# Kernel optimization log

Hardware: AMD Instinct MI355X
Metric: run time of the kernel (lower is better)

Reference implementation:

```python
import jax, jax.numpy as jnp
import numpy as np
import math

B, T, C, TF, N, DK = 4, 2048, 768, 128, 8, 96  # DK = max(C//8,16)

def _tau_init(Tw):
    alpha = 0.1 ** (1.0 / max(Tw - 1, 1))
    tau = -math.log(max(alpha, 1e-10))
    return math.log(math.exp(tau) - 1 + 1e-10)

def setup_inputs() -> dict:
    key = jax.random.key(0)
    ks = jax.random.split(key, 13)
    w = lambda k, shp: jax.random.normal(k, shp, jnp.float32) * 0.02
    return {
        'x': jax.random.normal(ks[0], (B, T, C), jnp.float32),
        'tau_gate': jnp.float32(_tau_init(max(T // 2, 4))),
        'tau_fast': jnp.float32(_tau_init(TF)),
        'tau_slow': jnp.float32(_tau_init(T)),
        'Wp': w(ks[1], (C, C)), 'bp': jnp.zeros((C,), jnp.float32),
        'Wxf': w(ks[2], (C, C)), 'bxf': jnp.full((C,), -0.5, jnp.float32),
        'Wxs': w(ks[3], (C, C)), 'bxs': jnp.full((C,), 0.5, jnp.float32),
        'Wcf': w(ks[4], (C, C)), 'Wcs': w(ks[5], (C, C)),
        'Wq': w(ks[6], (DK, C)), 'Wk': w(ks[7], (DK, C)),
        'Wfast': w(ks[8], (C, C)), 'bfast': jnp.zeros((C,), jnp.float32),
        'Wslow': w(ks[9], (C, C)), 'bslow': jnp.zeros((C,), jnp.float32),
        'Wsoma': w(ks[10], (C, C)), 'bsoma': jnp.zeros((C,), jnp.float32),
        'Wanc': w(ks[11], (C, C)), 'banc': jnp.zeros((C,), jnp.float32),
        'anchor_scales': jnp.linspace(1.5, -1.5, N).astype(jnp.float32),
        'blend_raw': jnp.zeros((1,), jnp.float32),
        'ln_g': jnp.ones((C,), jnp.float32), 'ln_b': jnp.zeros((C,), jnp.float32),
    }

def _lin(x, W, b=None):
    # torch Linear: y = x @ W.T + b, W is (out, in)
    y = jnp.einsum('btc,oc->bto', x, W)
    return y if b is None else y + b

def _ema(b, tau_raw):
    # exact h_t = alpha*h_{t-1} + b_t, h_{-1}=0 (same math as full causal conv with kernel alpha^j)
    alpha = jnp.exp(-jax.nn.softplus(tau_raw))
    def step(h, bt):
        h = alpha * h + bt
        return h, h
    _, hs = jax.lax.scan(step, jnp.zeros_like(b[:, 0, :]), jnp.swapaxes(b, 0, 1))
    return jnp.swapaxes(hs, 0, 1)  # (B,T,C)

def _forward(x, tau_gate, tau_fast, tau_slow, Wp, bp, Wxf, bxf, Wxs, bxs, Wcf, Wcs,
             Wq, Wk, Wfast, bfast, Wslow, bslow, Wsoma, bsoma, Wanc, banc,
             anchor_scales, blend_raw, ln_g, ln_b):
    x_proj = jnp.tanh(_lin(x, Wp, bp))
    ctx_gate = _ema(x, tau_gate)
    wg_f = jax.nn.sigmoid(_lin(x, Wxf, bxf) + _lin(ctx_gate, Wcf))
    wg_s = jax.nn.sigmoid(_lin(x, Wxs, bxs) + _lin(ctx_gate, Wcs))
    ctx_fast = _ema(x_proj * wg_f, tau_fast)
    ctx_slow = _ema(x_proj * wg_s, tau_slow)
    # F1 content gate: causal max-score sigmoid
    q = _lin(x, Wq)
    k = _lin(x, Wk)
    sc = jnp.einsum('btd,bsd->bts', q, k) * (DK ** -0.5)
    tril = jnp.tril(jnp.ones((T, T), bool))
    sc = jnp.where(tril[None], sc, -jnp.inf)
    cg = jax.nn.sigmoid(jnp.max(sc, axis=-1, keepdims=True))  # (B,T,1)
    ctx_fast = ctx_fast * cg
    ctx_slow = ctx_slow * cg
    # F5 anchors (static positions)
    pos = np.array([min(i * (T // N), T - 1) for i in range(N)])
    a = jnp.tanh(jnp.einsum('bnc,oc->bno', x[:, pos, :], Wanc) + banc)  # (B,N,C)
    delta = jnp.einsum('n,bnc->bc', jax.nn.sigmoid(anchor_scales), a)
    ctx_fast = ctx_fast + delta[:, None, :]
    ctx_slow = ctx_slow + delta[:, None, :]
    # F6 blend of fast/slow gates (torch.lerp)
    bl = jax.nn.sigmoid(blend_raw)  # (1,)
    gf = jax.nn.sigmoid(_lin(ctx_fast, Wfast, bfast))
    gs = jax.nn.sigmoid(_lin(ctx_slow, Wslow, bslow))
    gate = gf + bl * (gs - gf)
    soma = jnp.tanh(_lin(x, Wsoma, bsoma))
    y = soma * gate
    mu = jnp.mean(y, -1, keepdims=True)
    var = jnp.var(y, -1, keepdims=True)
    return (y - mu) / jnp.sqrt(var + 1e-5) * ln_g + ln_b  # dropout p=0 -> identity

def reference(x, tau_gate, tau_fast, tau_slow, Wp, bp, Wxf, bxf, Wxs, bxs, Wcf, Wcs,
              Wq, Wk, Wfast, bfast, Wslow, bslow, Wsoma, bsoma, Wanc, banc,
              anchor_scales, blend_raw, ln_g, ln_b):
    return _forward(x, tau_gate, tau_fast, tau_slow, Wp, bp, Wxf, bxf, Wxs, bxs, Wcf, Wcs,
                    Wq, Wk, Wfast, bfast, Wslow, bslow, Wsoma, bsoma, Wanc, banc,
                    anchor_scales, blend_raw, ln_g, ln_b)
```

## Files before the change

### kernel.cpp

```cpp
#include <hip/hip_runtime.h>
#include <math.h>

#define B_ 4
#define T_ 2048
#define C_ 768
#define DK_ 96
#define NA_ 8
#define M_ (B_*T_)
#define K2_ (2*C_)
#define NCH_ 256
#define CK_ 8

typedef __attribute__((ext_vector_type(8))) _Float16 half8;
typedef __attribute__((ext_vector_type(4))) _Float16 half4;
typedef __attribute__((ext_vector_type(4))) float floatx4;

#define AS1 __attribute__((address_space(1)))
#define AS3 __attribute__((address_space(3)))

__device__ __forceinline__ float sigm(float x){
  return __builtin_amdgcn_rcpf(1.f + __expf(-x));
}
__device__ __forceinline__ float ftanh(float x){
  return 1.f - 2.f*__builtin_amdgcn_rcpf(1.f + __expf(2.f*x));
}
__device__ __forceinline__ unsigned enc_max(float f){
  unsigned i = __float_as_uint(f);
  return (i & 0x80000000u) ? ~i : (i | 0x80000000u);
}
__device__ __forceinline__ float dec_max(unsigned u){
  unsigned i = (u & 0x80000000u) ? (u & 0x7FFFFFFFu) : ~u;
  return __uint_as_float(i);
}
__device__ __forceinline__ void gld16(const _Float16* g, _Float16* l){
  __builtin_amdgcn_global_load_lds((const AS1 unsigned int*)g, (AS3 unsigned int*)l, 16, 0, 0);
}

__device__ __forceinline__ void scan2l(const float* __restrict__ S, float* __restrict__ H,
                                       int b, int cg0, float aCK, float A16,
                                       float* __restrict__ carry ){
  int tid = threadIdx.x;
  int cl = tid & 15, g = tid >> 4;
  int c = cg0 + cl;
  float sv[16];
  float cv = 0.f;
  #pragma unroll
  for (int j = 0; j < 16; ++j){
    sv[j] = S[(size_t)(b*NCH_ + g*16 + j)*C_ + c];
    cv = aCK*cv + sv[j];
  }
  carry[cl*17 + g] = cv;
  __syncthreads();
  float h = 0.f;
  for (int gp = 0; gp < g; ++gp) h = A16*h + carry[cl*17 + gp];
  #pragma unroll
  for (int j = 0; j < 16; ++j){
    H[(size_t)(b*NCH_ + g*16 + j)*C_ + c] = h;
    h = aCK*h + sv[j];
  }
}

__global__ __launch_bounds__(192) void k_castx(
    const float* __restrict__ x, const float* __restrict__ tau,
    _Float16* __restrict__ xh, float* __restrict__ Sg){
  float al = expf(-log1pf(expf(tau[0])));
  int blk = blockIdx.x, b = blk >> 8, ch = blk & (NCH_-1);
  int t0 = b*T_ + ch*CK_;
  int c4 = threadIdx.x;
  float s0=0.f,s1=0.f,s2=0.f,s3=0.f;
  #pragma unroll
  for (int t = 0; t < CK_; ++t){
    float4 v = *(const float4*)(x + (size_t)(t0+t)*C_ + c4*4);
    half4 h = { (_Float16)v.x,(_Float16)v.y,(_Float16)v.z,(_Float16)v.w };
    *(half4*)(xh + (size_t)(t0+t)*C_ + c4*4) = h;
    s0 = al*s0 + v.x; s1 = al*s1 + v.y; s2 = al*s2 + v.z; s3 = al*s3 + v.w;
  }
  float4 sv = { s0,s1,s2,s3 };
  *(float4*)(Sg + (size_t)blk*C_ + c4*4) = sv;
}

#define NB0 4608
#define NB1 4896
#define NB2 4920
#define NB3 5112
__global__ __launch_bounds__(256) void k_prep(
    const float* __restrict__ x,
    const float* __restrict__ Wp, const float* __restrict__ Wfast,
    const float* __restrict__ Wslow, const float* __restrict__ Wsoma,
    const float* __restrict__ Wxf, const float* __restrict__ Wxs,
    const float* __restrict__ Wcf, const float* __restrict__ Wcs,
    const float* __restrict__ Wq, const float* __restrict__ Wk,
    const float* __restrict__ Wanc, const float* __restrict__ banc,
    const float* __restrict__ ascl, const float* __restrict__ tau_gate,
    const float* __restrict__ Sg,
    _Float16* __restrict__ wall, _Float16* __restrict__ wqk,
    unsigned* __restrict__ cgE, float* __restrict__ Hg, float* __restrict__ dlt)
{
  __shared__ float xs[NA_*C_];
  __shared__ float part[NA_*128];
  __shared__ float carry[16*17];
  int blk = blockIdx.x, tid = threadIdx.x;
  if (blk < NB0){
    int i = blk*256 + tid;
    const int per = (C_*C_)/4;
    int s = i / per, j = i - s*per;
    const float* src = s==0?Wp : s==1?Wfast : s==2?Wslow : s==3?Wsoma
                     : s==4?Wxf : s==5?Wxs : s==6?Wcf : Wcs;
    float4 v = ((const float4*)src)[j];
    half4 h = { (_Float16)v.x, (_Float16)v.y, (_Float16)v.z, (_Float16)v.w };
    ((half4*)wall)[(size_t)s*per + j] = h;
  } else if (blk < NB1){
    int sub = blk - NB0;
    if (sub >= 256){ cgE[(sub-256)*256 + tid] = 0u; return; }
    const float* src = (sub < 96) ? Wq + (size_t)sub*C_
                     : (sub < 192 ? Wk + (size_t)(sub-96)*C_ : nullptr);
    #pragma unroll
    for (int k = 0; k < 3; ++k){
      int c = tid + k*256;
      wqk[(size_t)sub*C_ + c] = src ? (_Float16)src[c] : (_Float16)0.f;
    }
  } else if (blk < NB2){
    int ab = blk - NB1;
    int ct = ab % 6, b = ab / 6;
    for (int i = tid; i < NA_*C_; i += 256){
      int n = i / C_, c = i - n*C_;
      xs[i] = x[(size_t)(b*T_ + n*(T_/NA_))*C_ + c];
    }
    __syncthreads();
    int col = ct*128 + (tid & 127), kh = tid >> 7;
    float acc[NA_] = {0,0,0,0,0,0,0,0};
    const float* wrow = Wanc + (size_t)col*C_ + kh*384;
    const float* xk = xs + kh*384;
    for (int k = 0; k < 384; ++k){
      float wv = wrow[k];
      #pragma unroll
      for (int n = 0; n < NA_; ++n) acc[n] += xk[n*C_ + k]*wv;
    }
    if (kh){
      #pragma unroll
      for (int n = 0; n < NA_; ++n) part[n*128 + (tid & 127)] = acc[n];
    }
    __syncthreads();
    if (!kh){
      float d = 0.f;
      float bv = banc[col];
      #pragma unroll
      for (int n = 0; n < NA_; ++n){
        float a = ftanh(acc[n] + part[n*128 + (tid & 127)] + bv);
        d += sigm(ascl[n]) * a;
      }
      dlt[(size_t)b*C_ + col] = d;
    }
  } else {
    int sub = blk - NB2;
    int b = sub / 48, cg0 = (sub - b*48)*16;
    float sp = log1pf(expf(tau_gate[0]));
    scan2l(Sg, Hg, b, cg0, expf(-8.f*sp), expf(-128.f*sp), carry);
  }
}

__global__ __launch_bounds__(256) void k_p2_fs(const float* __restrict__ Sf, const float* __restrict__ Ss,
                                               float* __restrict__ Hf, float* __restrict__ Hs,
                                               const float* __restrict__ tf, const float* __restrict__ ts){
  __shared__ float carry[16*17];
  int blk = blockIdx.x;
  int which = blk / (B_*48);
  int rem = blk - which*(B_*48);
  int b = rem / 48, cg0 = (rem - b*48)*16;
  float sp = log1pf(expf(which ? ts[0] : tf[0]));
  scan2l(which ? Ss : Sf, which ? Hs : Hf, b, cg0, expf(-8.f*sp), expf(-128.f*sp), carry);
}

__global__ __launch_bounds__(192) void k_gate_p3(
    const _Float16* __restrict__ xh, const float* __restrict__ H,
    const float* __restrict__ tau, _Float16* __restrict__ gate){
  float al = expf(-log1pf(expf(tau[0])));
  int tid = threadIdx.x;
  int half = tid / 96, ct = tid - half*96;
  int g = blockIdx.x*2 + half;
  int b = g >> 8, ch = g & (NCH_-1);
  int c0 = ct*8;
  int t0 = b*T_ + ch*CK_;
  float4 h0a = *(const float4*)(H + (size_t)g*C_ + c0);
  float4 h0b = *(const float4*)(H + (size_t)g*C_ + c0 + 4);
  float gv[8] = { h0a.x,h0a.y,h0a.z,h0a.w, h0b.x,h0b.y,h0b.z,h0b.w };
  #pragma unroll
  for (int t = 0; t < CK_; ++t){
    half8 v = *(const half8*)(xh + (size_t)(t0+t)*C_ + c0);
    half8 o;
    #pragma unroll
    for (int i = 0; i < 8; ++i){
      gv[i] = al*gv[i] + (float)v[i];
      o[i] = (_Float16)gv[i];
    }
    *(half8*)(gate + (size_t)(t0+t)*C_ + c0) = o;
  }
}

__global__ __launch_bounds__(192) void k_fs_p3(
    const _Float16* __restrict__ xph, _Float16* __restrict__ wgfs,
    const float* __restrict__ Hf, const float* __restrict__ Hs,
    const float* __restrict__ tf, const float* __restrict__ ts,
    const unsigned* __restrict__ cgE, const float* __restrict__ dlt){
  float af = expf(-log1pf(expf(tf[0])));
  float as = expf(-log1pf(expf(ts[0])));
  int tid = threadIdx.x;
  int half = tid / 96, ct = tid - half*96;
  int g = blockIdx.x*2 + half;
  int b = g >> 8, ch = g & (NCH_-1);
  int c0 = ct*8;
  int t0 = b*T_ + ch*CK_;
  float4 hfa = *(const float4*)(Hf + (size_t)g*C_ + c0);
  float4 hfb = *(const float4*)(Hf + (size_t)g*C_ + c0 + 4);
  float4 hsa = *(const float4*)(Hs + (size_t)g*C_ + c0);
  float4 hsb = *(const float4*)(Hs + (size_t)g*C_ + c0 + 4);
  float4 d4a = *(const float4*)(dlt + (size_t)b*C_ + c0);
  float4 d4b = *(const float4*)(dlt + (size_t)b*C_ + c0 + 4);
  float fv[8] = { hfa.x,hfa.y,hfa.z,hfa.w, hfb.x,hfb.y,hfb.z,hfb.w };
  float ev[8] = { hsa.x,hsa.y,hsa.z,hsa.w, hsb.x,hsb.y,hsb.z,hsb.w };
  float dv[8] = { d4a.x,d4a.y,d4a.z,d4a.w, d4b.x,d4b.y,d4b.z,d4b.w };
  float cgr[CK_];
  #pragma unroll
  for (int t = 0; t < CK_; ++t) cgr[t] = sigm(dec_max(cgE[t0+t]));
  #pragma unroll
  for (int t = 0; t < CK_; ++t){
    size_t rp = (size_t)(t0+t);
    half8 p  = *(const half8*)(xph  + rp*C_  + c0);
    half8 wf = *(const half8*)(wgfs + rp*K2_ + c0);
    half8 ws = *(const half8*)(wgfs + rp*K2_ + C_ + c0);
    float cg = cgr[t];
    half8 of, os;
    #pragma unroll
    for (int i = 0; i < 8; ++i){
      fv[i] = af*fv[i] + (float)p[i]*(float)wf[i];
      ev[i] = as*ev[i] + (float)p[i]*(float)ws[i];
      of[i] = (_Float16)(fv[i]*cg + dv[i]);
      os[i] = (_Float16)(ev[i]*cg + dv[i]);
    }
    *(half8*)(wgfs + rp*K2_ + c0) = of;
    *(half8*)(wgfs + rp*K2_ + C_ + c0) = os;
  }
}

__device__ __forceinline__ void stage_tile(const _Float16* __restrict__ src, int stride,
                                           int r0, int k0, _Float16* lds){
  int tid = threadIdx.x;
  int wave = tid >> 6, lane = tid & 63;
  #pragma unroll
  for (int it = 0; it < 4; ++it){
    int cb = it*256 + wave*64;
    int ck = cb + lane;
    int row = ck >> 3;
    int kp = (ck & 7) ^ (row & 7);
    gld16(src + (size_t)(r0+row)*stride + k0 + kp*8, lds + (size_t)cb*8);
  }
}

__device__ __forceinline__ void mfma_pass(const _Float16* As, const _Float16* Ws, floatx4 acc[4][4]){
  int tid = threadIdx.x;
  int wave = tid >> 6, lane = tid & 63;
  int wr = wave >> 1, wc = wave & 1;
  int lr = lane & 15, lq = lane >> 4;
  #pragma unroll
  for (int ks = 0; ks < 2; ++ks){
    half8 fa[4], fb[4];
    int off = (((ks*4 + lq) ^ (lr & 7)) << 3);
    #pragma unroll
    for (int i = 0; i < 4; ++i){
      fa[i] = *(const half8*)(As + (wr*64 + i*16 + lr)*64 + off);
      fb[i] = *(const half8*)(Ws + (wc*64 + i*16 + lr)*64 + off);
    }
    #pragma unroll
    for (int i = 0; i < 4; ++i)
      #pragma unroll
      for (int j = 0; j < 4; ++j)
        acc[i][j] = __builtin_amdgcn_mfma_f32_16x16x32_f16(fa[i], fb[j], acc[i][j], 0, 0, 0);
  }
}

__device__ __forceinline__ void store_tile_f16(floatx4 acc[4][4], _Float16* __restrict__ out, int ldo,
                                               const float* bias, const float* bias2,
                                               int m0, int n0, int act){
  int tid = threadIdx.x;
  int wave = tid >> 6, lane = tid & 63;
  int wr = wave >> 1, wc = wave & 1;
  int lr = lane & 15, lq = lane >> 4;
  #pragma unroll
  for (int i = 0; i < 4; ++i){
    #pragma unroll
    for (int j = 0; j < 4; ++j){
      int col = n0 + wc*64 + j*16 + lr;
      float bv = 0.f;
      if (bias) bv = (bias2 && col >= C_) ? bias2[col - C_] : bias[col];
      #pragma unroll
      for (int r = 0; r < 4; ++r){
        int rowm = m0 + wr*64 + i*16 + lq*4 + r;
        float z = acc[i][j][r] + bv;
        if (act == 1) z = ftanh(z);
        else if (act == 2) z = sigm(z);
        out[(size_t)rowm*ldo + col] = (_Float16)z;
      }
    }
  }
}

__global__ __launch_bounds__(256,4) void k_gemm_s3(
    const _Float16* __restrict__ xh, const _Float16* __restrict__ gate,
    const _Float16* __restrict__ wall, const _Float16* __restrict__ wqk,
    const float* __restrict__ bp, const float* __restrict__ bxf, const float* __restrict__ bxs,
    _Float16* __restrict__ xph, _Float16* __restrict__ wgfs, _Float16* __restrict__ qk)
{
  __shared__ _Float16 As[128*64];
  __shared__ _Float16 Ws[128*64];
  const size_t per = (size_t)C_*C_;
  floatx4 acc[4][4] = {};
  int m0 = blockIdx.x * 128;
  int ny = blockIdx.y;
  if (ny < 6){
    for (int k0 = 0; k0 < C_; k0 += 64){
      stage_tile(xh, C_, m0, k0, As);
      stage_tile(wall, C_, ny*128, k0, Ws);
      asm volatile("s_waitcnt vmcnt(0)" ::: "memory");
      __syncthreads();
      mfma_pass(As, Ws, acc);
      __syncthreads();
    }
    store_tile_f16(acc, xph, C_, bp, nullptr, m0, ny*128, 1);
  } else if (ny < 18){
    int n0 = (ny-6)*128;
    for (int k0 = 0; k0 < C_; k0 += 64){
      stage_tile(xh, C_, m0, k0, As);
      stage_tile(wall + 4*per, C_, n0, k0, Ws);
      asm volatile("s_waitcnt vmcnt(0)" ::: "memory");
      __syncthreads();
      mfma_pass(As, Ws, acc);
      __syncthreads();
    }
    for (int k0 = 0; k0 < C_; k0 += 64){
      stage_tile(gate, C_, m0, k0, As);
      stage_tile(wall + 6*per, C_, n0, k0, Ws);
      asm volatile("s_waitcnt vmcnt(0)" ::: "memory");
      __syncthreads();
      mfma_pass(As, Ws, acc);
      __syncthreads();
    }
    store_tile_f16(acc, wgfs, K2_, bxf, bxs, m0, n0, 2);
  } else {
    int n0 = (ny-18)*128;
    for (int k0 = 0; k0 < C_; k0 += 64){
      stage_tile(xh, C_, m0, k0, As);
      stage_tile(wqk, C_, n0, k0, Ws);
      asm volatile("s_waitcnt vmcnt(0)" ::: "memory");
      __syncthreads();
      mfma_pass(As, Ws, acc);
      __syncthreads();
    }
    store_tile_f16(acc, qk, 256, nullptr, nullptr, m0, n0, 0);
  }
}

__global__ __launch_bounds__(256,4) void k_gemm_s7(
    const _Float16* __restrict__ cfs, const _Float16* __restrict__ xh,
    const _Float16* __restrict__ wall,
    const float* __restrict__ bf, const float* __restrict__ bs, const float* __restrict__ bso,
    _Float16* __restrict__ gfb, _Float16* __restrict__ gsb, _Float16* __restrict__ somab)
{
  __shared__ _Float16 As[128*64];
  __shared__ _Float16 Bs[128*64];
  const size_t per = (size_t)C_*C_;
  floatx4 acc[4][4] = {};
  int m0 = blockIdx.x * 128;
  int s = blockIdx.y / 6, nt = (blockIdx.y % 6) * 128;
  const _Float16* Asrc = (s == 0) ? cfs : (s == 1 ? cfs + C_ : xh);
  int lda = (s == 2) ? C_ : K2_;
  const _Float16* Bsrc = wall + (size_t)(s+1)*per;
  for (int k0 = 0; k0 < C_; k0 += 64){
    stage_tile(Asrc, lda, m0, k0, As);
    stage_tile(Bsrc, C_, nt, k0, Bs);
    asm volatile("s_waitcnt vmcnt(0)" ::: "memory");
    __syncthreads();
    mfma_pass(As, Bs, acc);
    __syncthreads();
  }
  if (s == 2)      store_tile_f16(acc, somab, C_, bso, nullptr, m0, nt, 1);
  else if (s == 1) store_tile_f16(acc, gsb,  C_, bs,  nullptr, m0, nt, 2);
  else             store_tile_f16(acc, gfb,  C_, bf,  nullptr, m0, nt, 2);
}

#define SLDK 104
__global__ __launch_bounds__(256,3) void k_score_fs(
    const _Float16* __restrict__ qk, unsigned* __restrict__ cgE,
    const _Float16* __restrict__ xp, const _Float16* __restrict__ wgfs,
    const float* __restrict__ tf, const float* __restrict__ ts,
    float* __restrict__ Sf, float* __restrict__ Ss)
{
  __shared__ _Float16 Qs[128*SLDK];
  __shared__ _Float16 Ks[128*SLDK];
  __shared__ float sred[256];
  int idx = blockIdx.x;
  int tid = threadIdx.x;
  if (idx >= 544){
    if (tid >= 192) return;
    int half = tid / 96, ct = tid - half*96;
    int f = (idx - 544)*2 + half;
    float af = expf(-log1pf(expf(tf[0])));
    float as = expf(-log1pf(expf(ts[0])));
    int b = f >> 8, ch = f & (NCH_-1);
    int t0 = b*T_ + ch*CK_;
    int c0 = ct*8;
    float fv[8] = {0,0,0,0,0,0,0,0};
    float sv[8] = {0,0,0,0,0,0,0,0};
    #pragma unroll
    for (int t = 0; t < CK_; ++t){
      half8 p  = *(const half8*)(xp + (size_t)(t0+t)*C_ + c0);
      half8 wf = *(const half8*)(wgfs + (size_t)(t0+t)*K2_ + c0);
      half8 ws = *(const half8*)(wgfs + (size_t)(t0+t)*K2_ + C_ + c0);
      #pragma unroll
      for (int i = 0; i < 8; ++i){
        fv[i] = af*fv[i] + (float)p[i]*(float)wf[i];
        sv[i] = as*sv[i] + (float)p[i]*(float)ws[i];
      }
    }
    float4 fa = { fv[0],fv[1],fv[2],fv[3] }, fb = { fv[4],fv[5],fv[6],fv[7] };
    float4 sa = { sv[0],sv[1],sv[2],sv[3] }, sb = { sv[4],sv[5],sv[6],sv[7] };
    *(float4*)(Sf + (size_t)f*C_ + c0)     = fa;
    *(float4*)(Sf + (size_t)f*C_ + c0 + 4) = fb;
    *(float4*)(Ss + (size_t)f*C_ + c0)     = sa;
    *(float4*)(Ss + (size_t)f*C_ + c0 + 4) = sb;
    return;
  }
  int b = idx / 136;
  int p = idx - b*136;
  int ti = (int)((sqrtf(8.f*p + 1.f) - 1.f)*0.5f);
  while ((ti+1)*(ti+2)/2 <= p) ++ti;
  while (ti*(ti+1)/2 > p) --ti;
  int sj = p - ti*(ti+1)/2;

  const _Float16* qg = qk + (size_t)(b*T_ + ti*128)*256;
  const _Float16* kg = qk + (size_t)(b*T_ + sj*128)*256 + 96;
  #pragma unroll
  for (int r = 0; r < 6; ++r){
    int ci = tid + r*256;
    int row = ci / 12, kp = ci % 12;
    *(uint4*)(&Qs[row*SLDK + kp*8]) = *(const uint4*)(qg + (size_t)row*256 + kp*8);
    *(uint4*)(&Ks[row*SLDK + kp*8]) = *(const uint4*)(kg + (size_t)row*256 + kp*8);
  }
  __syncthreads();

  int wave = tid >> 6, lane = tid & 63;
  int wr = wave >> 1, wc = wave & 1;
  int lr = lane & 15, lq = lane >> 4;
  floatx4 acc[4][4] = {};
  #pragma unroll
  for (int ks = 0; ks < 3; ++ks){
    half8 fa[4], fb[4];
    #pragma unroll
    for (int i = 0; i < 4; ++i){
      fa[i] = *(const half8*)(&Qs[(wr*64 + i*16 + lr)*SLDK + ks*32 + lq*8]);
      fb[i] = *(const half8*)(&Ks[(wc*64 + i*16 + lr)*SLDK + ks*32 + lq*8]);
    }
    #pragma unroll
    for (int i = 0; i < 4; ++i)
      #pragma unroll
      for (int j = 0; j < 4; ++j)
        acc[i][j] = __builtin_amdgcn_mfma_f32_16x16x32_f16(fa[i], fb[j], acc[i][j], 0, 0, 0);
  }
  const float scale = 0.10206207f;
  #pragma unroll
  for (int i = 0; i < 4; ++i){
    #pragma unroll
    for (int r = 0; r < 4; ++r){
      int row64 = i*16 + lq*4 + r;
      int tg = ti*128 + wr*64 + row64;
      float v = -3.0e38f;
      #pragma unroll
      for (int j = 0; j < 4; ++j){
        int sg = sj*128 + wc*64 + j*16 + lr;
        if (sg <= tg) v = fmaxf(v, acc[i][j][r]*scale);
      }
      #pragma unroll
      for (int off = 1; off < 16; off <<= 1) v = fmaxf(v, __shfl_xor(v, off, 16));
      if (lr == 0) sred[wr*128 + wc*64 + row64] = v;
    }
  }
  __syncthreads();
  if (wc == 0 && lane < 64){
    int row64 = lane;
    float v = fmaxf(sred[wr*128 + row64], sred[wr*128 + 64 + row64]);
    int tg = ti*128 + wr*64 + row64;
    atomicMax(&cgE[(size_t)b*T_ + tg], enc_max(v));
  }
}

__global__ __launch_bounds__(256) void k_ln(const _Float16* __restrict__ gfb,
                                            const _Float16* __restrict__ gsb,
                                            const _Float16* __restrict__ somab,
                                            const float* __restrict__ blendr,
                                            const float* __restrict__ g, const float* __restrict__ be,
                                            float* __restrict__ out){
  int wave = threadIdx.x >> 6, lane = threadIdx.x & 63;
  int half = lane >> 5, l32 = lane & 31;
  int row = blockIdx.x*8 + wave*2 + half;
  float bl = sigm(blendr[0]);
  size_t rb = (size_t)row*C_;
  float v[24];
  float s = 0.f, ss = 0.f;
  #pragma unroll
  for (int w2 = 0; w2 < 3; ++w2){
    size_t o = rb + w2*256 + l32*8;
    half8 gf8 = *(const half8*)(gfb + o);
    half8 gs8 = *(const half8*)(gsb + o);
    half8 so8 = *(const half8*)(somab + o);
    #pragma unroll
    for (int i = 0; i < 8; ++i){
      float gf = (float)gf8[i], gs = (float)gs8[i], so = (float)so8[i];
      float y = so * (gf + bl*(gs - gf));
      v[w2*8 + i] = y; s += y; ss += y*y;
    }
  }
  #pragma unroll
  for (int off = 1; off < 32; off <<= 1){ s += __shfl_xor(s, off, 32); ss += __shfl_xor(ss, off, 32); }
  float mu  = s * (1.f/C_);
  float var = ss * (1.f/C_) - mu*mu;
  float inv = rsqrtf(var + 1e-5f);
  #pragma unroll
  for (int w2 = 0; w2 < 3; ++w2){
    int c0 = w2*256 + l32*8;
    float4 oa, ob;
    oa.x = (v[w2*8+0]-mu)*inv*g[c0+0] + be[c0+0];
    oa.y = (v[w2*8+1]-mu)*inv*g[c0+1] + be[c0+1];
    oa.z = (v[w2*8+2]-mu)*inv*g[c0+2] + be[c0+2];
    oa.w = (v[w2*8+3]-mu)*inv*g[c0+3] + be[c0+3];
    ob.x = (v[w2*8+4]-mu)*inv*g[c0+4] + be[c0+4];
    ob.y = (v[w2*8+5]-mu)*inv*g[c0+5] + be[c0+5];
    ob.z = (v[w2*8+6]-mu)*inv*g[c0+6] + be[c0+6];
    ob.w = (v[w2*8+7]-mu)*inv*g[c0+7] + be[c0+7];
    *(float4*)(out + rb + c0)     = oa;
    *(float4*)(out + rb + c0 + 4) = ob;
  }
}

extern "C" void kernel_launch(void* const* d_in, const int* in_sizes, int n_in,
                              void* d_out, int out_size, void* d_ws, size_t ws_size,
                              hipStream_t stream){
  (void)in_sizes; (void)n_in; (void)out_size;
  const float* x        = (const float*)d_in[0];
  const float* tau_gate = (const float*)d_in[1];
  const float* tau_fast = (const float*)d_in[2];
  const float* tau_slow = (const float*)d_in[3];
  const float* Wp   = (const float*)d_in[4];  const float* bp    = (const float*)d_in[5];
  const float* Wxf  = (const float*)d_in[6];  const float* bxf   = (const float*)d_in[7];
  const float* Wxs  = (const float*)d_in[8];  const float* bxs   = (const float*)d_in[9];
  const float* Wcf  = (const float*)d_in[10]; const float* Wcs   = (const float*)d_in[11];
  const float* Wq   = (const float*)d_in[12]; const float* Wk    = (const float*)d_in[13];
  const float* Wfast= (const float*)d_in[14]; const float* bfast = (const float*)d_in[15];
  const float* Wslow= (const float*)d_in[16]; const float* bslow = (const float*)d_in[17];
  const float* Wsoma= (const float*)d_in[18]; const float* bsoma = (const float*)d_in[19];
  const float* Wanc = (const float*)d_in[20]; const float* banc  = (const float*)d_in[21];
  const float* ascl = (const float*)d_in[22]; const float* blendr= (const float*)d_in[23];
  const float* lng  = (const float*)d_in[24]; const float* lnb   = (const float*)d_in[25];
  float* out = (float*)d_out;

  char* w = (char*)d_ws;
  auto alloc = [&](size_t bytes)->void*{
    void* p = (void*)w; w += (bytes + 255) & ~(size_t)255; return p;
  };
  _Float16* xh    = (_Float16*)alloc((size_t)M_*C_*2);
  _Float16* wall  = (_Float16*)alloc((size_t)8*C_*C_*2);
  _Float16* wqk   = (_Float16*)alloc((size_t)256*C_*2);
  _Float16* xph   = (_Float16*)alloc((size_t)M_*C_*2);
  _Float16* wgfs  = (_Float16*)alloc((size_t)M_*K2_*2);
  _Float16* qk    = (_Float16*)alloc((size_t)M_*256*2);
  _Float16* gfb   = (_Float16*)alloc((size_t)M_*C_*2);
  _Float16* gsb   = (_Float16*)alloc((size_t)M_*C_*2);
  _Float16* somab = (_Float16*)alloc((size_t)M_*C_*2);
  unsigned* cgE   = (unsigned*)alloc((size_t)M_*4);
  float* Sg = (float*)alloc((size_t)B_*NCH_*C_*4);
  float* Hg = (float*)alloc((size_t)B_*NCH_*C_*4);
  float* Ss = (float*)alloc((size_t)B_*NCH_*C_*4);
  float* Hs = (float*)alloc((size_t)B_*NCH_*C_*4);
  float* dlt = (float*)alloc((size_t)B_*C_*4);
  _Float16* gate = gfb;
  float* Sf = Sg;
  float* Hf = Hg;
  if ((size_t)(w - (char*)d_ws) > ws_size) return;

  k_castx<<<B_*NCH_, 192, 0, stream>>>(x, tau_gate, xh, Sg);
  k_prep<<<NB3, 256, 0, stream>>>(x, Wp, Wfast, Wslow, Wsoma, Wxf, Wxs, Wcf, Wcs, Wq, Wk,
                                  Wanc, banc, ascl, tau_gate, Sg, wall, wqk, cgE, Hg, dlt);
  k_gate_p3<<<B_*NCH_/2, 192, 0, stream>>>(xh, Hg, tau_gate, gate);
  k_gemm_s3<<<dim3(M_/128, 20), 256, 0, stream>>>(xh, gate, wall, wqk,
                                                  bp, bxf, bxs, xph, wgfs, qk);
  k_score_fs<<<544 + B_*NCH_/2, 256, 0, stream>>>(qk, cgE, xph, wgfs, tau_fast, tau_slow, Sf, Ss);
  k_p2_fs<<<2*B_*48, 256, 0, stream>>>(Sf, Ss, Hf, Hs, tau_fast, tau_slow);
  k_fs_p3<<<B_*NCH_/2, 192, 0, stream>>>(xph, wgfs, Hf, Hs, tau_fast, tau_slow, cgE, dlt);
  k_gemm_s7<<<dim3(M_/128, 18), 256, 0, stream>>>(wgfs, xh, wall,
                                                  bfast, bslow, bsoma, gfb, gsb, somab);
  k_ln<<<M_/8, 256, 0, stream>>>(gfb, gsb, somab, blendr, lng, lnb, out);
}
```

Before: 318.4 us.

## Fuse fast/slow/soma GEMMs with gate blend into one kernel writing y

Each block now runs the fast, slow and soma GEMMs in sequence for one output tile, keeps the sigmoid gates in registers, blends them, multiplies by tanh(soma) and writes a single fp16 y array. LayerNorm then reads one array instead of three. This removes two intermediate fp16 buffers' writes and reads, but the grid drops to a third as many blocks, and the register-held gates raise pressure, which may hurt occupancy and load balance.

```diff
diff --git a/kernel.cpp b/kernel.cpp
--- a/kernel.cpp
+++ b/kernel.cpp
@@ -359,32 +359,94 @@
   }
 }
 
-__global__ __launch_bounds__(256,4) void k_gemm_s7(
+__global__ __launch_bounds__(256,4) void k_gemm_s7y(
     const _Float16* __restrict__ cfs, const _Float16* __restrict__ xh,
     const _Float16* __restrict__ wall,
     const float* __restrict__ bf, const float* __restrict__ bs, const float* __restrict__ bso,
-    _Float16* __restrict__ gfb, _Float16* __restrict__ gsb, _Float16* __restrict__ somab)
+    const float* __restrict__ blendr, _Float16* __restrict__ y)
 {
   __shared__ _Float16 As[128*64];
   __shared__ _Float16 Bs[128*64];
   const size_t per = (size_t)C_*C_;
-  floatx4 acc[4][4] = {};
-  int m0 = blockIdx.x * 128;
-  int s = blockIdx.y / 6, nt = (blockIdx.y % 6) * 128;
-  const _Float16* Asrc = (s == 0) ? cfs : (s == 1 ? cfs + C_ : xh);
-  int lda = (s == 2) ? C_ : K2_;
-  const _Float16* Bsrc = wall + (size_t)(s+1)*per;
-  for (int k0 = 0; k0 < C_; k0 += 64){
-    stage_tile(Asrc, lda, m0, k0, As);
-    stage_tile(Bsrc, C_, nt, k0, Bs);
-    asm volatile("s_waitcnt vmcnt(0)" ::: "memory");
-    __syncthreads();
-    mfma_pass(As, Bs, acc);
-    __syncthreads();
-  }
-  if (s == 2)      store_tile_f16(acc, somab, C_, bso, nullptr, m0, nt, 1);
-  else if (s == 1) store_tile_f16(acc, gsb,  C_, bs,  nullptr, m0, nt, 2);
-  else             store_tile_f16(acc, gfb,  C_, bf,  nullptr, m0, nt, 2);
+  int m0 = blockIdx.x * 128, nt = blockIdx.y * 128;
+  int tid = threadIdx.x;
+  int wave = tid >> 6, lane = tid & 63;
+  int wr = wave >> 1, wc = wave & 1;
+  int lr = lane & 15, lq = lane >> 4;
+  float bl = sigm(blendr[0]);
+  half4 gp[4][4];
+
+  {
+    floatx4 acc[4][4] = {};
+    for (int k0 = 0; k0 < C_; k0 += 64){
+      stage_tile(cfs, K2_, m0, k0, As);
+      stage_tile(wall + 1*per, C_, nt, k0, Bs);
+      asm volatile("s_waitcnt vmcnt(0)" ::: "memory");
+      __syncthreads();
+      mfma_pass(As, Bs, acc);
+      __syncthreads();
+    }
+    #pragma unroll
+    for (int i = 0; i < 4; ++i)
+      #pragma unroll
+      for (int j = 0; j < 4; ++j){
+        float bv = bf[nt + wc*64 + j*16 + lr];
+        half4 h;
+        #pragma unroll
+        for (int r = 0; r < 4; ++r) h[r] = (_Float16)sigm(acc[i][j][r] + bv);
+        gp[i][j] = h;
+      }
+  }
+  {
+    floatx4 acc[4][4] = {};
+    for (int k0 = 0; k0 < C_; k0 += 64){
+      stage_tile(cfs + C_, K2_, m0, k0, As);
+      stage_tile(wall + 2*per, C_, nt, k0, Bs);
+      asm volatile("s_waitcnt vmcnt(0)" ::: "memory");
+      __syncthreads();
+      mfma_pass(As, Bs, acc);
+      __syncthreads();
+    }
+    #pragma unroll
+    for (int i = 0; i < 4; ++i)
+      #pragma unroll
+      for (int j = 0; j < 4; ++j){
+        float bv = bs[nt + wc*64 + j*16 + lr];
+        half4 h = gp[i][j];
+        #pragma unroll
+        for (int r = 0; r < 4; ++r){
+          float gf = (float)h[r];
+          float gs = sigm(acc[i][j][r] + bv);
+          h[r] = (_Float16)(gf + bl*(gs - gf));
+        }
+        gp[i][j] = h;
+      }
+  }
+  {
+    floatx4 acc[4][4] = {};
+    for (int k0 = 0; k0 < C_; k0 += 64){
+      stage_tile(xh, C_, m0, k0, As);
+      stage_tile(wall + 3*per, C_, nt, k0, Bs);
+      asm volatile("s_waitcnt vmcnt(0)" ::: "memory");
+      __syncthreads();
+      mfma_pass(As, Bs, acc);
+      __syncthreads();
+    }
+    #pragma unroll
+    for (int i = 0; i < 4; ++i)
+      #pragma unroll
+      for (int j = 0; j < 4; ++j){
+        int col = nt + wc*64 + j*16 + lr;
+        float bv = bso[col];
+        half4 h = gp[i][j];
+        #pragma unroll
+        for (int r = 0; r < 4; ++r){
+          int rowm = m0 + wr*64 + i*16 + lq*4 + r;
+          float z = ftanh(acc[i][j][r] + bv) * (float)h[r];
+          y[(size_t)rowm*C_ + col] = (_Float16)z;
+        }
+      }
+  }
 }
 
 #define SLDK 104
@@ -492,30 +554,23 @@
   }
 }
 
-__global__ __launch_bounds__(256) void k_ln(const _Float16* __restrict__ gfb,
-                                            const _Float16* __restrict__ gsb,
-                                            const _Float16* __restrict__ somab,
-                                            const float* __restrict__ blendr,
+__global__ __launch_bounds__(256) void k_ln(const _Float16* __restrict__ yb,
                                             const float* __restrict__ g, const float* __restrict__ be,
                                             float* __restrict__ out){
   int wave = threadIdx.x >> 6, lane = threadIdx.x & 63;
   int half = lane >> 5, l32 = lane & 31;
   int row = blockIdx.x*8 + wave*2 + half;
-  float bl = sigm(blendr[0]);
   size_t rb = (size_t)row*C_;
   float v[24];
   float s = 0.f, ss = 0.f;
   #pragma unroll
   for (int w2 = 0; w2 < 3; ++w2){
     size_t o = rb + w2*256 + l32*8;
-    half8 gf8 = *(const half8*)(gfb + o);
-    half8 gs8 = *(const half8*)(gsb + o);
-    half8 so8 = *(const half8*)(somab + o);
+    half8 y8 = *(const half8*)(yb + o);
     #pragma unroll
     for (int i = 0; i < 8; ++i){
-      float gf = (float)gf8[i], gs = (float)gs8[i], so = (float)so8[i];
-      float y = so * (gf + bl*(gs - gf));
-      v[w2*8 + i] = y; s += y; ss += y*y;
+      float yv = (float)y8[i];
+      v[w2*8 + i] = yv; s += yv; ss += yv*yv;
     }
   }
   #pragma unroll
@@ -571,16 +626,14 @@
   _Float16* xph   = (_Float16*)alloc((size_t)M_*C_*2);
   _Float16* wgfs  = (_Float16*)alloc((size_t)M_*K2_*2);
   _Float16* qk    = (_Float16*)alloc((size_t)M_*256*2);
-  _Float16* gfb   = (_Float16*)alloc((size_t)M_*C_*2);
-  _Float16* gsb   = (_Float16*)alloc((size_t)M_*C_*2);
-  _Float16* somab = (_Float16*)alloc((size_t)M_*C_*2);
+  _Float16* yb    = (_Float16*)alloc((size_t)M_*C_*2);
   unsigned* cgE   = (unsigned*)alloc((size_t)M_*4);
   float* Sg = (float*)alloc((size_t)B_*NCH_*C_*4);
   float* Hg = (float*)alloc((size_t)B_*NCH_*C_*4);
   float* Ss = (float*)alloc((size_t)B_*NCH_*C_*4);
   float* Hs = (float*)alloc((size_t)B_*NCH_*C_*4);
   float* dlt = (float*)alloc((size_t)B_*C_*4);
-  _Float16* gate = gfb;
+  _Float16* gate = yb;
   float* Sf = Sg;
   float* Hf = Hg;
   if ((size_t)(w - (char*)d_ws) > ws_size) return;
@@ -594,7 +647,7 @@
   k_score_fs<<<544 + B_*NCH_/2, 256, 0, stream>>>(qk, cgE, xph, wgfs, tau_fast, tau_slow, Sf, Ss);
   k_p2_fs<<<2*B_*48, 256, 0, stream>>>(Sf, Ss, Hf, Hs, tau_fast, tau_slow);
   k_fs_p3<<<B_*NCH_/2, 192, 0, stream>>>(xph, wgfs, Hf, Hs, tau_fast, tau_slow, cgE, dlt);
-  k_gemm_s7<<<dim3(M_/128, 18), 256, 0, stream>>>(wgfs, xh, wall,
-                                                  bfast, bslow, bsoma, gfb, gsb, somab);
-  k_ln<<<M_/8, 256, 0, stream>>>(gfb, gsb, somab, blendr, lng, lnb, out);
-}
+  k_gemm_s7y<<<dim3(M_/128, 6), 256, 0, stream>>>(wgfs, xh, wall,
+                                                  bfast, bslow, bsoma, blendr, yb);
+  k_ln<<<M_/8, 256, 0, stream>>>(yb, lng, lnb, out);
+}
```

Measured after the change: 407.1 us. 1.28x slower.
